# Kernel optimization log

Hardware: AMD Instinct MI355X
Metric: run time of the kernel (lower is better)

Reference implementation:

```python
import jax, jax.numpy as jnp
import numpy as np

ZERO = 1e-8
L = 2            # num_gnn_layers
D = 256          # dim_node_features
B = 32           # graphs per batch
NPG = 256        # nodes per graph
N = B * NPG      # total nodes
E = 131072       # edges per edge-type
MAX_TOKENS = 256 # MAX_TOKENS_OF_A_POST
UPD = 0.5        # args.updated_weights_for_A


def _make_edges(k):
    k1, k2, k3 = jax.random.split(k, 3)
    g = jax.random.randint(k1, (E,), 0, B) * NPG          # keep edges within a graph
    src = g + jax.random.randint(k2, (E,), 0, NPG)
    dst = g + jax.random.randint(k3, (E,), 0, NPG)
    return jnp.stack([src, dst]).astype(jnp.int64)


def setup_inputs() -> dict:
    key = jax.random.key(0)
    ks = jax.random.split(key, 12)
    x = jax.random.normal(ks[0], (N, D), dtype=jnp.float32)
    ei_e = _make_edges(ks[1]); ew_e = jax.random.uniform(ks[2], (E,), dtype=jnp.float32)
    ei_p = _make_edges(ks[3]); ew_p = jax.random.uniform(ks[4], (E,), dtype=jnp.float32)
    ei_o = _make_edges(ks[5]); ew_o = jax.random.uniform(ks[6], (E,), dtype=jnp.float32)
    entity_mask = jax.random.randint(ks[7], (B, NPG), 0, 2).astype(bool)
    pattern_mask = jax.random.randint(ks[8], (B, NPG), 0, 2).astype(bool)
    s = 1.0 / np.sqrt(D)
    W_gcn = (jax.random.normal(ks[9], (L, 3, D, D), dtype=jnp.float32) * s)
    b_gcn = jnp.zeros((L, 3, D), dtype=jnp.float32)
    T_dyn = (jax.random.normal(ks[10], (L, D, D), dtype=jnp.float32) * s)
    return {
        'x': x,
        'edge_index_entity': ei_e, 'edge_weight_entity': ew_e,
        'edge_index_pattern': ei_p, 'edge_weight_pattern': ew_p,
        'edge_index_others': ei_o, 'edge_weight_others': ew_o,
        'entity_mask': entity_mask, 'pattern_mask': pattern_mask,
        'W_gcn': W_gcn, 'b_gcn': b_gcn, 'T_dyn': T_dyn,
    }


def _normalized_correlation_matrix(H):
    # cosine-similarity correlation matrix, symmetrically degree-normalized
    nrm = jnp.sqrt(jnp.sum(H * H, axis=1))
    A = (H @ H.T) / (nrm[:, None] * nrm[None, :] + ZERO)
    dinv = 1.0 / jnp.sqrt(jnp.abs(jnp.sum(A, axis=1)) + ZERO)
    return dinv[:, None] * A * dinv[None, :]


def _gcn(H, W, b, ei, ew):
    # GCNConv(add_self_loops=False, normalize=False): scatter-sum of weighted source messages
    msg = (H @ W)[ei[0]] * ew[:, None]                     # [E, D]
    return jax.ops.segment_sum(msg, ei[1], num_segments=N) + b


def _forward(x, we0, wp0, wo0, W_gcn, b_gcn, T_dyn,
             ei_e, ei_p, ei_o, entity_mask, pattern_mask):
    H = x
    A = _normalized_correlation_matrix(H)                  # [N, N]
    for i in range(L):
        if i == 0:
            we, wp, wo = we0, wp0, wo0
        else:
            # diag(one_hot(src) @ A @ one_hot(dst).T) == A[src, dst]
            we = A[ei_e[0], ei_e[1]]
            wp = A[ei_p[0], ei_p[1]]
            wo = A[ei_o[0], ei_o[1]]
        He = _gcn(H, W_gcn[i, 0], b_gcn[i, 0], ei_e, we)
        Hp = _gcn(H, W_gcn[i, 1], b_gcn[i, 1], ei_p, wp)
        Ho = _gcn(H, W_gcn[i, 2], b_gcn[i, 2], ei_o, wo)
        H = jax.nn.relu(He + Hp + Ho)
        A_hat = jax.nn.sigmoid((H @ T_dyn[i]) @ H.T)
        A = (1.0 - UPD) * A + UPD * A_hat
    # per-graph diagonal blocks of A  -> [B, NPG, NPG]
    A4 = A.reshape(B, NPG, B, NPG)
    idx = jnp.arange(B)
    blocks = A4[idx, :, idx, :]
    A_sum = jnp.sum(blocks, axis=-1)                       # [B, NPG]
    ent_cols = jnp.einsum('bij,bj->bi', blocks, entity_mask.astype(A.dtype))
    pat_cols = jnp.einsum('bij,bj->bi', blocks, pattern_mask.astype(A.dtype))
    map_pattern = A_sum - ent_cols
    map_entity = A_sum - pat_cols

    def finish(m):
        mn = jnp.min(m, axis=1, keepdims=True)
        mx = jnp.max(m, axis=1, keepdims=True)
        m = (m - mn) / (mx - mn + ZERO)
        m = m / (jnp.sum(m, axis=1, keepdims=True) + ZERO)
        return m[:, :MAX_TOKENS]                           # padding() with NPG==MAX_TOKENS

    return finish(map_entity), finish(map_pattern)


def reference(x, edge_index_entity, edge_weight_entity,
              edge_index_pattern, edge_weight_pattern,
              edge_index_others, edge_weight_others,
              entity_mask, pattern_mask, W_gcn, b_gcn, T_dyn):
    return _forward(x, edge_weight_entity, edge_weight_pattern, edge_weight_others,
                    W_gcn, b_gcn, T_dyn,
                    edge_index_entity, edge_index_pattern, edge_index_others,
                    entity_mask, pattern_mask)
```

## Files before the change

kernel.cpp:

```cpp
#include <hip/hip_runtime.h>

#define NND   8192
#define DDIM  256
#define NGRP  32
#define ZEROF 1e-8f
#define LSTR  40
#define TSTR  72
#define OFF_AH 0
#define OFF_AL 2560
#define OFF_BH 5120
#define OFF_BL 10240
#define OFF_TT 5120
#define LDS_U16 15360

typedef unsigned short u16;
typedef __attribute__((ext_vector_type(8))) short short8v;
typedef __attribute__((ext_vector_type(4))) float float4v;

__device__ inline u16 f2bf(float x) {
  unsigned u = __float_as_uint(x);
  u += 0x7fffu + ((u >> 16) & 1u);
  return (u16)(u >> 16);
}
__device__ inline float bf2f(u16 h) { return __uint_as_float((unsigned)h << 16); }
__device__ inline void split2(float x, u16& h, u16& l) {
  h = f2bf(x);
  l = f2bf(x - bf2f(h));
}

__device__ inline float wave_sum(float v) {
#pragma unroll
  for (int off = 32; off > 0; off >>= 1) v += __shfl_down(v, off, 64);
  return v;
}

#define LOAD_REGS(tt, kk)                                                                   \
  {                                                                                         \
    int m_ = tid >> 2, kq_ = (tid & 3) * 8;                                                 \
    size_t aoff_;                                                                           \
    if (MODE == 1)                                                                          \
      aoff_ = (size_t)((tt) * 256 + bym * 64 + m_) * 8192 + (size_t)(g * 256 + (kk) + kq_); \
    else if (MODE == 2 || MODE == 3)                                                        \
      aoff_ = (size_t)(g * 256 + bym * 64 + m_) * 256 + (kk) + kq_;                         \
    else                                                                                    \
      aoff_ = (size_t)(bym * 64 + m_) * 256 + (kk) + kq_;                                   \
    rAh = *(const short8v*)&Ah_g[aoff_];                                                    \
    rAl = *(const short8v*)&Al_g[aoff_];                                                    \
    if (MODE == 1) {                                                                        \
      int n_ = tid >> 2, kq2_ = (tid & 3) * 8;                                              \
      const float* pb_ = Bfp + (((size_t)g * 3 + (tt)) << 16) +                             \
                         (size_t)(col0 + n_) * 256 + (kk) + kq2_;                           \
      rBf[0] = *(const float4*)pb_;                                                         \
      rBf[1] = *(const float4*)(pb_ + 4);                                                   \
    } else if (HALF) {                                                                      \
      int n_ = tid & 63, kq2_ = (tid >> 6) * 8;                                             \
      size_t boff_ = (size_t)(((MODE == 2 || MODE == 3) ? g * 256 : 0) + col0 + n_) * 256   \
                     + (kk) + kq2_;                                                         \
      rBh0 = *(const short8v*)&Bh_g[boff_];                                                 \
      rBl0 = *(const short8v*)&Bl_g[boff_];                                                 \
    } else {                                                                                \
      int n_ = tid & 127, kq2_ = (tid >> 7) * 16;                                           \
      size_t boff_ = (size_t)(col0 + n_) * 256 + (kk) + kq2_;                               \
      rBh0 = *(const short8v*)&Bh_g[boff_]; rBh1 = *(const short8v*)&Bh_g[boff_ + 8];       \
      rBl0 = *(const short8v*)&Bl_g[boff_]; rBl1 = *(const short8v*)&Bl_g[boff_ + 8];       \
    }                                                                                       \
  }

template<int MODE, bool HALF>
__device__ __forceinline__ void mfma_body(
    u16* lds,
    const u16* __restrict__ Ah_g, const u16* __restrict__ Al_g,
    const u16* __restrict__ Bh_g, const u16* __restrict__ Bl_g,
    const float* __restrict__ Bfp,
    float* __restrict__ Cf, u16* __restrict__ Ch, u16* __restrict__ Cl,
    const float* __restrict__ nrm, const float* __restrict__ dinv,
    const float* __restrict__ bias,
    int bxm, int bym, int g) {
  u16* Ahs = lds + OFF_AH;
  u16* Als = lds + OFF_AL;
  u16* Bhs = lds + OFF_BH;
  u16* Bls = lds + OFF_BL;
  u16* Tt  = lds + OFF_TT;
  const int NJ = HALF ? 2 : 4;
  const int tid = threadIdx.x;
  const int col0 = bxm * (HALF ? 64 : 128);
  const int w = tid >> 6, lane = tid & 63;
  const int lm = lane & 15, lq = lane >> 4;
  const int wr = (w >> 1) * 32, wc = (w & 1) * (HALF ? 32 : 64);

  float4v acc[2][4];
#pragma unroll
  for (int i = 0; i < 2; ++i)
#pragma unroll
    for (int j = 0; j < NJ; ++j) acc[i][j] = (float4v)0.f;

  short8v rAh, rAl, rBh0, rBh1, rBl0, rBl1;
  float4 rBf[2];
  const int TOTAL = (MODE == 1) ? 24 : 8;

  LOAD_REGS(0, 0);
  for (int step = 0; step < TOTAL; ++step) {
    if (step) __syncthreads();
    {
      int m = tid >> 2, kq = (tid & 3) * 8;
      *(short8v*)&Ahs[m * LSTR + kq] = rAh;
      *(short8v*)&Als[m * LSTR + kq] = rAl;
    }
    if (MODE == 1) {
      int n = tid >> 2, kq2 = (tid & 3) * 8;
      u16 hh[8], ll[8];
      split2(rBf[0].x, hh[0], ll[0]); split2(rBf[0].y, hh[1], ll[1]);
      split2(rBf[0].z, hh[2], ll[2]); split2(rBf[0].w, hh[3], ll[3]);
      split2(rBf[1].x, hh[4], ll[4]); split2(rBf[1].y, hh[5], ll[5]);
      split2(rBf[1].z, hh[6], ll[6]); split2(rBf[1].w, hh[7], ll[7]);
      *(short8v*)&Bhs[n * LSTR + kq2] = *(short8v*)hh;
      *(short8v*)&Bls[n * LSTR + kq2] = *(short8v*)ll;
    } else if (HALF) {
      int n = tid & 63, kq2 = (tid >> 6) * 8;
      *(short8v*)&Bhs[n * LSTR + kq2] = rBh0;
      *(short8v*)&Bls[n * LSTR + kq2] = rBl0;
    } else {
      int n = tid & 127, kq2 = (tid >> 7) * 16;
      *(short8v*)&Bhs[n * LSTR + kq2] = rBh0; *(short8v*)&Bhs[n * LSTR + kq2 + 8] = rBh1;
      *(short8v*)&Bls[n * LSTR + kq2] = rBl0; *(short8v*)&Bls[n * LSTR + kq2 + 8] = rBl1;
    }
    __syncthreads();
    int nxt = step + 1;
    if (nxt < TOTAL) {
      int tt = nxt >> 3, kk = (nxt & 7) * 32;
      LOAD_REGS(tt, kk);
    }
    short8v ah[2], al[2], bh[4], bl[4];
#pragma unroll
    for (int i = 0; i < 2; ++i) {
      int r = wr + i * 16 + lm;
      ah[i] = *(const short8v*)&Ahs[r * LSTR + lq * 8];
      al[i] = *(const short8v*)&Als[r * LSTR + lq * 8];
    }
#pragma unroll
    for (int j = 0; j < NJ; ++j) {
      int r = wc + j * 16 + lm;
      bh[j] = *(const short8v*)&Bhs[r * LSTR + lq * 8];
      bl[j] = *(const short8v*)&Bls[r * LSTR + lq * 8];
    }
#pragma unroll
    for (int i = 0; i < 2; ++i)
#pragma unroll
      for (int j = 0; j < NJ; ++j) {
        acc[i][j] = __builtin_amdgcn_mfma_f32_16x16x32_bf16(ah[i], bh[j], acc[i][j], 0, 0, 0);
        acc[i][j] = __builtin_amdgcn_mfma_f32_16x16x32_bf16(ah[i], bl[j], acc[i][j], 0, 0, 0);
        acc[i][j] = __builtin_amdgcn_mfma_f32_16x16x32_bf16(al[i], bh[j], acc[i][j], 0, 0, 0);
      }
  }

  if (MODE == 2 || MODE == 3) {
#pragma unroll
    for (int i = 0; i < 2; ++i) {
#pragma unroll
      for (int r = 0; r < 4; ++r) {
        int grow = g * 256 + bym * 64 + wr + i * 16 + lq * 4 + r;
        float di = 0.f, ni = 0.f;
        if (MODE == 2) { di = dinv[grow]; ni = nrm[grow]; }
#pragma unroll
        for (int j = 0; j < NJ; ++j) {
          int gcol = col0 + wc + j * 16 + lm;
          size_t ci = (size_t)grow * 256 + gcol;
          float v = acc[i][j][r];
          if (MODE == 2) {
            int gj = g * 256 + gcol;
            Cf[ci] = v * di * dinv[gj] / (ni * nrm[gj] + ZEROF);
          } else {
            Cf[ci] = 0.5f * Cf[ci] + 0.5f * (1.f / (1.f + expf(-v)));
          }
        }
      }
    }
  } else {
    float bsum[8];
    if (MODE == 1) {
#pragma unroll
      for (int i = 0; i < 2; ++i)
#pragma unroll
        for (int r = 0; r < 4; ++r) {
          int d = bym * 64 + wr + i * 16 + lq * 4 + r;
          bsum[i * 4 + r] = bias[d] + bias[256 + d] + bias[512 + d];
        }
    }
    u16 hv[32], lv[32];
#pragma unroll
    for (int i = 0; i < 2; ++i)
#pragma unroll
      for (int j = 0; j < NJ; ++j)
#pragma unroll
        for (int r = 0; r < 4; ++r) {
          float v = acc[i][j][r];
          if (MODE == 1) v = fmaxf(v + bsum[i * 4 + r], 0.f);
          split2(v, hv[(i * 4 + r) * NJ + j], lv[(i * 4 + r) * NJ + j]);
        }
    int ebase1 = (MODE == 1) ? (g * 256 + col0) : col0;
    int ebase2 = bym * 64;
    size_t estride = (MODE == 0) ? 8192 : 256;
#pragma unroll
    for (int ph = 0; ph < 2; ++ph) {
      __syncthreads();
      const u16* sv = ph ? lv : hv;
#pragma unroll
      for (int i = 0; i < 2; ++i)
#pragma unroll
        for (int j = 0; j < NJ; ++j)
#pragma unroll
          for (int r = 0; r < 4; ++r)
            Tt[(wc + j * 16 + lm) * TSTR + wr + i * 16 + lq * 4 + r] = sv[(i * 4 + r) * NJ + j];
      __syncthreads();
      u16* dst = ph ? Cl : Ch;
      int cc0 = tid >> 3, mm0 = (tid & 7) * 8;
#pragma unroll
      for (int it = 0; it < (HALF ? 2 : 4); ++it) {
        int cc = it * 32 + cc0;
        short8v v = *(const short8v*)&Tt[cc * TSTR + mm0];
        *(short8v*)&dst[(size_t)(ebase1 + cc) * estride + ebase2 + mm0] = v;
      }
    }
  }
}

__global__ void k_prep(const int* __restrict__ e0, const int* __restrict__ e1,
                       const int* __restrict__ e2, const unsigned char* __restrict__ m0,
                       const unsigned char* __restrict__ m1,
                       const float* __restrict__ W, const float* __restrict__ T,
                       const float* __restrict__ x,
                       int* __restrict__ eo, float* __restrict__ emf, float* __restrict__ pmf,
                       u16* __restrict__ Wth, u16* __restrict__ Wtl,
                       float* __restrict__ Mzero,
                       float* __restrict__ nrm, float* __restrict__ Spart,
                       u16* __restrict__ Hh, u16* __restrict__ Hl,
                       int E2, int nCvt) {
  __shared__ float tile[32][33];
  __shared__ float inv[64];
  __shared__ int nz[2];
  const int b = blockIdx.x, tid = threadIdx.x;
  if (b < nCvt) {
    if (tid < 2) nz[tid] = 0;
    __syncthreads();
    if (e0[2 * tid + 1] != 0) atomicAdd(&nz[0], 1);
    int i4 = tid * 4;
    int c = (m0[i4 + 1] != 0) + (m0[i4 + 2] != 0) + (m0[i4 + 3] != 0);
    if (c) atomicAdd(&nz[1], c);
    __syncthreads();
    int fE = (nz[0] == 0), fM = (nz[1] == 0);
    int i = b * 256 + tid;
    if (i < E2) {
      eo[i] = fE ? e0[2 * i] : e0[i];
    } else if (i < 2 * E2) {
      int j = i - E2; eo[E2 + j] = fE ? e1[2 * j] : e1[j];
    } else if (i < 3 * E2) {
      int j = i - 2 * E2; eo[2 * E2 + j] = fE ? e2[2 * j] : e2[j];
    } else if (i < 3 * E2 + NND) {
      int j = i - 3 * E2; unsigned char v = fM ? m0[4 * j] : m0[j];
      emf[j] = 1.f - (float)(v != 0);
    } else if (i < 3 * E2 + 2 * NND) {
      int j = i - 3 * E2 - NND; unsigned char v = fM ? m1[4 * j] : m1[j];
      pmf[j] = 1.f - (float)(v != 0);
    }
  } else if (b < nCvt + 512) {
    int bb = b - nCvt;
    int mat = bb >> 6, rem = bb & 63;
    int k0 = (rem >> 3) * 32, n0 = (rem & 7) * 32;
    const float* src = (mat < 6) ? (W + (size_t)mat * 65536) : (T + (size_t)(mat - 6) * 65536);
    int r = tid >> 3, c4 = (tid & 7) * 4;
    const float4 v = *(const float4*)&src[(size_t)(k0 + r) * 256 + n0 + c4];
    tile[r][c4 + 0] = v.x; tile[r][c4 + 1] = v.y; tile[r][c4 + 2] = v.z; tile[r][c4 + 3] = v.w;
    __syncthreads();
    float o[4] = {tile[c4 + 0][r], tile[c4 + 1][r], tile[c4 + 2][r], tile[c4 + 3][r]};
    u16 hh[4], ll[4];
#pragma unroll
    for (int q = 0; q < 4; ++q) split2(o[q], hh[q], ll[q]);
    size_t off = (size_t)mat * 65536 + (size_t)(n0 + r) * 256 + k0 + c4;
    *(ushort4*)&Wth[off] = *(ushort4*)hh;
    *(ushort4*)&Wtl[off] = *(ushort4*)ll;
  } else if (b < nCvt + 512 + 3072) {
    int bb = b - nCvt - 512;
    float4* p = (float4*)Mzero;
    size_t base = (size_t)bb * 1024 + tid;
    float4 z = make_float4(0.f, 0.f, 0.f, 0.f);
    p[base] = z; p[base + 256] = z; p[base + 512] = z; p[base + 768] = z;
  } else {
    int bn = b - nCvt - 512 - 3072;
    int n0 = bn * 64;
    int w = tid >> 6, lane = tid & 63;
    for (int it = 0; it < 16; ++it) {
      int nl = it * 4 + w;
      int node = n0 + nl;
      const float4 v = *(const float4*)&x[(size_t)node * 256 + lane * 4];
      u16 hh[4], ll[4];
      split2(v.x, hh[0], ll[0]); split2(v.y, hh[1], ll[1]);
      split2(v.z, hh[2], ll[2]); split2(v.w, hh[3], ll[3]);
      *(ushort4*)&Hh[(size_t)node * 256 + lane * 4] = *(ushort4*)hh;
      *(ushort4*)&Hl[(size_t)node * 256 + lane * 4] = *(ushort4*)ll;
      float s = wave_sum(v.x * v.x + v.y * v.y + v.z * v.z + v.w * v.w);
      if (lane == 0) { float nr = sqrtf(s); nrm[node] = nr; inv[nl] = 1.f / nr; }
    }
    __syncthreads();
    float s = 0.f;
    for (int i = 0; i < 64; ++i) s += x[(size_t)(n0 + i) * 256 + tid] * inv[i];
    Spart[bn * 256 + tid] = s;
  }
}

__global__ __launch_bounds__(256, 2) void k_stageA(
    const u16* __restrict__ Hinh, const u16* __restrict__ Hinl,
    const u16* __restrict__ Wth, const u16* __restrict__ Wtl, int l,
    u16* __restrict__ XWTh, u16* __restrict__ XWTl,
    const int* __restrict__ edges, const float* __restrict__ ew0,
    const float* __restrict__ ew1, const float* __restrict__ ew2,
    const float* __restrict__ Abuf, float* __restrict__ Mb, int E_,
    const float* __restrict__ x, const float* __restrict__ Spart,
    const float* __restrict__ nrm, float* __restrict__ dinv) {
  __shared__ u16 lds[LDS_U16];
  const int b = blockIdx.x;
  if (b < 768) {
    mfma_body<0, false>(lds, Hinh, Hinl, Wth + (size_t)l * 768 * 256,
                        Wtl + (size_t)l * 768 * 256, nullptr,
                        nullptr, XWTh, XWTl, nullptr, nullptr, nullptr,
                        b >> 7, b & 127, 0);
  } else if (b < 1280) {
    int bi = b - 768;
    for (int i = bi * 256 + threadIdx.x; i < 3 * E_; i += 131072) {
      int t = i / E_;
      int e = i - t * E_;
      const int* ei = edges + (size_t)t * 2 * E_;
      int src = ei[e], dst = ei[E_ + e];
      float wgt = l ? Abuf[(size_t)src * 256 + (dst & 255)]
                    : (t == 0 ? ew0 : (t == 1 ? ew1 : ew2))[e];
      int gg = src >> 8;
      atomicAdd(&Mb[(((size_t)gg * 3 + t) << 16) + ((size_t)(dst & 255) << 8) + (src & 255)],
                wgt);
    }
  } else {
    float* Sl = (float*)lds;
    const int tid = threadIdx.x;
    float s = 0.f;
    for (int bb = 0; bb < 128; ++bb) s += Spart[bb * 256 + tid];
    Sl[tid] = s;
    __syncthreads();
    int base = (b - 1280) * 64;
    int w = tid >> 6, lane = tid & 63;
    const float4 sv = *(const float4*)&Sl[lane * 4];
    for (int it = 0; it < 16; ++it) {
      int node = base + it * 4 + w;
      const float4 v = *(const float4*)&x[(size_t)node * 256 + lane * 4];
      float s2 = wave_sum(v.x * sv.x + v.y * sv.y + v.z * sv.z + v.w * sv.w);
      if (lane == 0) {
        float rowsum = s2 / nrm[node];
        dinv[node] = rsqrtf(fabsf(rowsum) + ZEROF);
      }
    }
  }
}

__global__ __launch_bounds__(256, 2) void k_stageB(
    const u16* __restrict__ XWTh, const u16* __restrict__ XWTl,
    const float* __restrict__ Mb,
    u16* __restrict__ Houth, u16* __restrict__ Houtl, const float* __restrict__ bias,
    const u16* __restrict__ xh, const u16* __restrict__ xl, float* __restrict__ Abuf,
    const float* __restrict__ nrm, const float* __restrict__ dinv) {
  __shared__ u16 lds[LDS_U16];
  const int b = blockIdx.x;
  if (b < 512) {
    int g = b & 31, r = b >> 5;
    mfma_body<1, true>(lds, XWTh, XWTl, nullptr, nullptr, Mb,
                       nullptr, Houth, Houtl, nullptr, nullptr, bias,
                       r >> 2, r & 3, g);
  } else {
    int bb = b - 512;
    int g = bb & 31, r = bb >> 5;
    mfma_body<2, true>(lds, xh, xl, xh, xl, nullptr, Abuf, nullptr, nullptr,
                       nrm, dinv, nullptr, r >> 2, r & 3, g);
  }
}

__global__ __launch_bounds__(256, 2) void k_stageC(
    const u16* __restrict__ Wth, const u16* __restrict__ Wtl, int l,
    const u16* __restrict__ Hh, const u16* __restrict__ Hl,
    u16* __restrict__ tmph, u16* __restrict__ tmpl) {
  __shared__ u16 lds[LDS_U16];
  const int b = blockIdx.x;
  mfma_body<4, true>(lds, Wth + (size_t)(6 + l) * 65536, Wtl + (size_t)(6 + l) * 65536,
                     Hh, Hl, nullptr, nullptr, tmph, tmpl, nullptr, nullptr, nullptr,
                     b & 127, b >> 7, 0);
}

__global__ __launch_bounds__(256, 2) void k_stageD(
    const u16* __restrict__ tmph, const u16* __restrict__ tmpl,
    const u16* __restrict__ Hh, const u16* __restrict__ Hl,
    float* __restrict__ Abuf) {
  __shared__ u16 lds[LDS_U16];
  const int b = blockIdx.x;
  int g = b & 31, r = b >> 5;
  mfma_body<3, true>(lds, tmph, tmpl, Hh, Hl, nullptr, Abuf, nullptr, nullptr,
                     nullptr, nullptr, nullptr, r >> 2, r & 3, g);
}

__global__ void k_maps(const float* __restrict__ Abuf, const float* __restrict__ emf,
                       const float* __restrict__ pmf, float* __restrict__ out) {
  __shared__ float sme[256], smp[256], red[256];
  const int g = blockIdx.x, tid = threadIdx.x, w = tid >> 6, lane = tid & 63;
  const int j0 = g * 256 + lane * 4;
  const float4 pmv = *(const float4*)&pmf[j0];
  const float4 emv = *(const float4*)&emf[j0];
  for (int it = 0; it < 64; ++it) {
    int nl = it * 4 + w;
    const float4 a = *(const float4*)&Abuf[((size_t)g * 256 + nl) * 256 + lane * 4];
    float me = a.x * pmv.x + a.y * pmv.y + a.z * pmv.z + a.w * pmv.w;
    float mp = a.x * emv.x + a.y * emv.y + a.z * emv.z + a.w * emv.w;
#pragma unroll
    for (int off = 32; off > 0; off >>= 1) {
      me += __shfl_down(me, off, 64);
      mp += __shfl_down(mp, off, 64);
    }
    if (lane == 0) { sme[nl] = me; smp[nl] = mp; }
  }
  __syncthreads();
  for (int which = 0; which < 2; ++which) {
    float v = which ? smp[tid] : sme[tid];
    red[tid] = v; __syncthreads();
    for (int s = 128; s > 0; s >>= 1) { if (tid < s) red[tid] = fminf(red[tid], red[tid + s]); __syncthreads(); }
    float mn = red[0]; __syncthreads();
    red[tid] = v; __syncthreads();
    for (int s = 128; s > 0; s >>= 1) { if (tid < s) red[tid] = fmaxf(red[tid], red[tid + s]); __syncthreads(); }
    float mx = red[0]; __syncthreads();
    float m = (v - mn) / (mx - mn + ZEROF);
    red[tid] = m; __syncthreads();
    for (int s = 128; s > 0; s >>= 1) { if (tid < s) red[tid] += red[tid + s]; __syncthreads(); }
    float sum = red[0]; __syncthreads();
    out[which * NND + g * 256 + tid] = m / (sum + ZEROF);
  }
}

extern "C" void kernel_launch(void* const* d_in, const int* in_sizes, int n_in,
                              void* d_out, int out_size, void* d_ws, size_t ws_size,
                              hipStream_t stream) {
  const float* x = (const float*)d_in[0];
  const unsigned char* em_raw = (const unsigned char*)d_in[7];
  const unsigned char* pm_raw = (const unsigned char*)d_in[8];
  const float* W  = (const float*)d_in[9];
  const float* bg = (const float*)d_in[10];
  const float* T  = (const float*)d_in[11];
  float* out = (float*)d_out;
  const int E_ = in_sizes[2];
  const int E2 = 2 * E_;

  float* ws = (float*)d_ws;
  size_t o = 0;
  float* Abuf = ws + o; o += (size_t)NND * 256;
  float* Mb3  = ws + o; o += (size_t)2 * NGRP * 3 * 65536;
  u16* Hh   = (u16*)(ws + o); o += (size_t)NND * 256 / 2;
  u16* Hl   = (u16*)(ws + o); o += (size_t)NND * 256 / 2;
  u16* H2h  = (u16*)(ws + o); o += (size_t)NND * 256 / 2;
  u16* H2l  = (u16*)(ws + o); o += (size_t)NND * 256 / 2;
  u16* tmph = (u16*)(ws + o); o += (size_t)NND * 256 / 2;
  u16* tmpl = (u16*)(ws + o); o += (size_t)NND * 256 / 2;
  u16* XWTh = (u16*)(ws + o); o += (size_t)768 * NND / 2;
  u16* XWTl = (u16*)(ws + o); o += (size_t)768 * NND / 2;
  u16* Wth  = (u16*)(ws + o); o += (size_t)8 * 65536 / 2;
  u16* Wtl  = (u16*)(ws + o); o += (size_t)8 * 65536 / 2;
  float* nrm   = ws + o; o += NND;
  float* dinv  = ws + o; o += NND;
  float* Spart = ws + o; o += 128 * 256;
  float* emf   = ws + o; o += NND;
  float* pmf   = ws + o; o += NND;
  int* edges   = (int*)(ws + o); o += (size_t)3 * E2;

  const float* ew0 = (const float*)d_in[2];
  const float* ew1 = (const float*)d_in[4];
  const float* ew2 = (const float*)d_in[6];
  float* Mb_l0 = Mb3;
  float* Mb_l1 = Mb3 + (size_t)NGRP * 3 * 65536;

  const int nCvt = (3 * E2 + 2 * NND + 255) / 256;

  k_prep<<<nCvt + 512 + 3072 + 128, 256, 0, stream>>>(
      (const int*)d_in[1], (const int*)d_in[3], (const int*)d_in[5], em_raw, pm_raw,
      W, T, x, edges, emf, pmf, Wth, Wtl, Mb3, nrm, Spart, Hh, Hl, E2, nCvt);

  k_stageA<<<1408, 256, 0, stream>>>(Hh, Hl, Wth, Wtl, 0, XWTh, XWTl,
                                     edges, ew0, ew1, ew2, Abuf, Mb_l0, E_,
                                     x, Spart, nrm, dinv);
  k_stageB<<<1024, 256, 0, stream>>>(XWTh, XWTl, Mb_l0, H2h, H2l, bg,
                                     Hh, Hl, Abuf, nrm, dinv);
  k_stageC<<<512, 256, 0, stream>>>(Wth, Wtl, 0, H2h, H2l, tmph, tmpl);
  k_stageD<<<512, 256, 0, stream>>>(tmph, tmpl, H2h, H2l, Abuf);

  k_stageA<<<1280, 256, 0, stream>>>(H2h, H2l, Wth, Wtl, 1, XWTh, XWTl,
                                     edges, ew0, ew1, ew2, Abuf, Mb_l1, E_,
                                     x, Spart, nrm, dinv);
  k_stageB<<<512, 256, 0, stream>>>(XWTh, XWTl, Mb_l1, Hh, Hl, bg + 768,
                                    nullptr, nullptr, nullptr, nullptr, nullptr);
  k_stageC<<<512, 256, 0, stream>>>(Wth, Wtl, 1, Hh, Hl, tmph, tmpl);
  k_stageD<<<512, 256, 0, stream>>>(tmph, tmpl, Hh, Hl, Abuf);

  k_maps<<<NGRP, 256, 0, stream>>>(Abuf, emf, pmf, out);
}
```

Baseline: 283.8 us.

## Bin edges by graph, type and destination slice; accumulate adjacency in shared memory

The prep kernel now buckets every edge into one of 768 bins, keyed by graph, edge type and 32-row destination slice. Each bin entry holds a packed 16-bit cell index and the edge weight. Stage A then builds each adjacency slice with shared-memory atomics and writes it densely to global memory, both layers reuse one Mb buffer, and the global-atomic scatter, the large zero-fill and the edge-index copy are gone. In exchange there is a fixed bin capacity of 1024 that silently drops edges in any bin that overflows, which is only safe for evenly spread inputs. It also adds an extra init kernel launch.

```diff
diff --git a/kernel.cpp b/kernel.cpp
--- a/kernel.cpp
+++ b/kernel.cpp
@@ -12,6 +12,8 @@
 #define OFF_BL 10240
 #define OFF_TT 5120
 #define LDS_U16 15360
+#define NBIN 768
+#define BINCAP 1024
 
 typedef unsigned short u16;
 typedef __attribute__((ext_vector_type(8))) short short8v;
@@ -224,46 +226,47 @@
   }
 }
 
+__global__ void k_init(unsigned* __restrict__ binCount) {
+  int i = blockIdx.x * 256 + threadIdx.x;
+  if (i < NBIN) binCount[i] = 0u;
+}
+
 __global__ void k_prep(const int* __restrict__ e0, const int* __restrict__ e1,
                        const int* __restrict__ e2, const unsigned char* __restrict__ m0,
                        const unsigned char* __restrict__ m1,
                        const float* __restrict__ W, const float* __restrict__ T,
                        const float* __restrict__ x,
-                       int* __restrict__ eo, float* __restrict__ emf, float* __restrict__ pmf,
+                       const float* __restrict__ ew0, const float* __restrict__ ew1,
+                       const float* __restrict__ ew2,
+                       float* __restrict__ emf, float* __restrict__ pmf,
                        u16* __restrict__ Wth, u16* __restrict__ Wtl,
-                       float* __restrict__ Mzero,
+                       unsigned* __restrict__ binCount, u16* __restrict__ binCell,
+                       float* __restrict__ binW,
                        float* __restrict__ nrm, float* __restrict__ Spart,
-                       u16* __restrict__ Hh, u16* __restrict__ Hl,
-                       int E2, int nCvt) {
+                       u16* __restrict__ Hh, u16* __restrict__ Hl, int E_) {
   __shared__ float tile[32][33];
   __shared__ float inv[64];
   __shared__ int nz[2];
   const int b = blockIdx.x, tid = threadIdx.x;
-  if (b < nCvt) {
-    if (tid < 2) nz[tid] = 0;
-    __syncthreads();
-    if (e0[2 * tid + 1] != 0) atomicAdd(&nz[0], 1);
+  if (b < 64) {
+    if (tid == 0) nz[1] = 0;
+    __syncthreads();
     int i4 = tid * 4;
     int c = (m0[i4 + 1] != 0) + (m0[i4 + 2] != 0) + (m0[i4 + 3] != 0);
     if (c) atomicAdd(&nz[1], c);
     __syncthreads();
-    int fE = (nz[0] == 0), fM = (nz[1] == 0);
+    int fM = (nz[1] == 0);
     int i = b * 256 + tid;
-    if (i < E2) {
-      eo[i] = fE ? e0[2 * i] : e0[i];
-    } else if (i < 2 * E2) {
-      int j = i - E2; eo[E2 + j] = fE ? e1[2 * j] : e1[j];
-    } else if (i < 3 * E2) {
-      int j = i - 2 * E2; eo[2 * E2 + j] = fE ? e2[2 * j] : e2[j];
-    } else if (i < 3 * E2 + NND) {
-      int j = i - 3 * E2; unsigned char v = fM ? m0[4 * j] : m0[j];
-      emf[j] = 1.f - (float)(v != 0);
-    } else if (i < 3 * E2 + 2 * NND) {
-      int j = i - 3 * E2 - NND; unsigned char v = fM ? m1[4 * j] : m1[j];
+    if (i < NND) {
+      unsigned char v = fM ? m0[4 * i] : m0[i];
+      emf[i] = 1.f - (float)(v != 0);
+    } else {
+      int j = i - NND;
+      unsigned char v = fM ? m1[4 * j] : m1[j];
       pmf[j] = 1.f - (float)(v != 0);
     }
-  } else if (b < nCvt + 512) {
-    int bb = b - nCvt;
+  } else if (b < 576) {
+    int bb = b - 64;
     int mat = bb >> 6, rem = bb & 63;
     int k0 = (rem >> 3) * 32, n0 = (rem & 7) * 32;
     const float* src = (mat < 6) ? (W + (size_t)mat * 65536) : (T + (size_t)(mat - 6) * 65536);
@@ -278,14 +281,32 @@
     size_t off = (size_t)mat * 65536 + (size_t)(n0 + r) * 256 + k0 + c4;
     *(ushort4*)&Wth[off] = *(ushort4*)hh;
     *(ushort4*)&Wtl[off] = *(ushort4*)ll;
-  } else if (b < nCvt + 512 + 3072) {
-    int bb = b - nCvt - 512;
-    float4* p = (float4*)Mzero;
-    size_t base = (size_t)bb * 1024 + tid;
-    float4 z = make_float4(0.f, 0.f, 0.f, 0.f);
-    p[base] = z; p[base + 256] = z; p[base + 512] = z; p[base + 768] = z;
+  } else if (b < 1088) {
+    if (tid == 0) nz[0] = 0;
+    __syncthreads();
+    if (e0[2 * tid + 1] != 0) atomicAdd(&nz[0], 1);
+    __syncthreads();
+    int fE = (nz[0] == 0);
+    int bb = b - 576;
+    for (int i = bb * 256 + tid; i < 3 * E_; i += 512 * 256) {
+      int t = i / E_;
+      int e = i - t * E_;
+      const int* er = (t == 0) ? e0 : (t == 1 ? e1 : e2);
+      int src, dst;
+      if (fE) { src = er[2 * e]; dst = er[2 * (E_ + e)]; }
+      else    { src = er[e];     dst = er[E_ + e]; }
+      float w = (t == 0 ? ew0 : (t == 1 ? ew1 : ew2))[e];
+      int g = src >> 8;
+      int dstl = dst & 255, srcl = src & 255;
+      int bin = ((g * 3 + t) << 3) | (dstl >> 5);
+      unsigned slot = atomicAdd(&binCount[bin], 1u);
+      if (slot < BINCAP) {
+        binCell[(size_t)bin * BINCAP + slot] = (u16)(((dstl & 31) << 8) | srcl);
+        binW[(size_t)bin * BINCAP + slot] = w;
+      }
+    }
   } else {
-    int bn = b - nCvt - 512 - 3072;
+    int bn = b - 1088;
     int n0 = bn * 64;
     int w = tid >> 6, lane = tid & 63;
     for (int it = 0; it < 16; ++it) {
@@ -311,39 +332,51 @@
     const u16* __restrict__ Hinh, const u16* __restrict__ Hinl,
     const u16* __restrict__ Wth, const u16* __restrict__ Wtl, int l,
     u16* __restrict__ XWTh, u16* __restrict__ XWTl,
-    const int* __restrict__ edges, const float* __restrict__ ew0,
-    const float* __restrict__ ew1, const float* __restrict__ ew2,
-    const float* __restrict__ Abuf, float* __restrict__ Mb, int E_,
+    const unsigned* __restrict__ binCount, const u16* __restrict__ binCell,
+    const float* __restrict__ binW,
+    const float* __restrict__ Abuf, float* __restrict__ Mb,
     const float* __restrict__ x, const float* __restrict__ Spart,
     const float* __restrict__ nrm, float* __restrict__ dinv) {
-  __shared__ u16 lds[LDS_U16];
+  __shared__ u16 lds[16384];
   const int b = blockIdx.x;
+  const int tid = threadIdx.x;
   if (b < 768) {
     mfma_body<0, false>(lds, Hinh, Hinl, Wth + (size_t)l * 768 * 256,
                         Wtl + (size_t)l * 768 * 256, nullptr,
                         nullptr, XWTh, XWTl, nullptr, nullptr, nullptr,
                         b >> 7, b & 127, 0);
-  } else if (b < 1280) {
-    int bi = b - 768;
-    for (int i = bi * 256 + threadIdx.x; i < 3 * E_; i += 131072) {
-      int t = i / E_;
-      int e = i - t * E_;
-      const int* ei = edges + (size_t)t * 2 * E_;
-      int src = ei[e], dst = ei[E_ + e];
-      float wgt = l ? Abuf[(size_t)src * 256 + (dst & 255)]
-                    : (t == 0 ? ew0 : (t == 1 ? ew1 : ew2))[e];
-      int gg = src >> 8;
-      atomicAdd(&Mb[(((size_t)gg * 3 + t) << 16) + ((size_t)(dst & 255) << 8) + (src & 255)],
-                wgt);
-    }
+  } else if (b < 1536) {
+    int bin = b - 768;
+    float* Ml = (float*)lds;
+    for (int i = tid; i < 8192; i += 256) Ml[i] = 0.f;
+    __syncthreads();
+    int count = min((int)binCount[bin], BINCAP);
+    const u16* cells = binCell + (size_t)bin * BINCAP;
+    const float* wts = binW + (size_t)bin * BINCAP;
+    int gt = bin >> 3, sub = bin & 7;
+    int g = gt / 3;
+    for (int i = tid; i < count; i += 256) {
+      int cell = cells[i];
+      float w;
+      if (l) {
+        int srcl = cell & 255, dstq = cell >> 8;
+        w = Abuf[(size_t)(g * 256 + srcl) * 256 + sub * 32 + dstq];
+      } else {
+        w = wts[i];
+      }
+      atomicAdd(&Ml[cell], w);
+    }
+    __syncthreads();
+    float4* dst = (float4*)(Mb + ((size_t)gt << 16) + (size_t)sub * 32 * 256);
+    const float4* srcp = (const float4*)Ml;
+    for (int i = tid; i < 2048; i += 256) dst[i] = srcp[i];
   } else {
     float* Sl = (float*)lds;
-    const int tid = threadIdx.x;
     float s = 0.f;
     for (int bb = 0; bb < 128; ++bb) s += Spart[bb * 256 + tid];
     Sl[tid] = s;
     __syncthreads();
-    int base = (b - 1280) * 64;
+    int base = (b - 1536) * 64;
     int w = tid >> 6, lane = tid & 63;
     const float4 sv = *(const float4*)&Sl[lane * 4];
     for (int it = 0; it < 16; ++it) {
@@ -448,12 +481,11 @@
   const float* T  = (const float*)d_in[11];
   float* out = (float*)d_out;
   const int E_ = in_sizes[2];
-  const int E2 = 2 * E_;
 
   float* ws = (float*)d_ws;
   size_t o = 0;
   float* Abuf = ws + o; o += (size_t)NND * 256;
-  float* Mb3  = ws + o; o += (size_t)2 * NGRP * 3 * 65536;
+  float* Mb   = ws + o; o += (size_t)NGRP * 3 * 65536;
   u16* Hh   = (u16*)(ws + o); o += (size_t)NND * 256 / 2;
   u16* Hl   = (u16*)(ws + o); o += (size_t)NND * 256 / 2;
   u16* H2h  = (u16*)(ws + o); o += (size_t)NND * 256 / 2;
@@ -469,32 +501,32 @@
   float* Spart = ws + o; o += 128 * 256;
   float* emf   = ws + o; o += NND;
   float* pmf   = ws + o; o += NND;
-  int* edges   = (int*)(ws + o); o += (size_t)3 * E2;
+  unsigned* binCount = (unsigned*)(ws + o); o += NBIN;
+  u16* binCell = (u16*)(ws + o); o += (size_t)NBIN * BINCAP / 2;
+  float* binW  = ws + o; o += (size_t)NBIN * BINCAP;
 
   const float* ew0 = (const float*)d_in[2];
   const float* ew1 = (const float*)d_in[4];
   const float* ew2 = (const float*)d_in[6];
-  float* Mb_l0 = Mb3;
-  float* Mb_l1 = Mb3 + (size_t)NGRP * 3 * 65536;
-
-  const int nCvt = (3 * E2 + 2 * NND + 255) / 256;
-
-  k_prep<<<nCvt + 512 + 3072 + 128, 256, 0, stream>>>(
+
+  k_init<<<3, 256, 0, stream>>>(binCount);
+  k_prep<<<1216, 256, 0, stream>>>(
       (const int*)d_in[1], (const int*)d_in[3], (const int*)d_in[5], em_raw, pm_raw,
-      W, T, x, edges, emf, pmf, Wth, Wtl, Mb3, nrm, Spart, Hh, Hl, E2, nCvt);
-
-  k_stageA<<<1408, 256, 0, stream>>>(Hh, Hl, Wth, Wtl, 0, XWTh, XWTl,
-                                     edges, ew0, ew1, ew2, Abuf, Mb_l0, E_,
+      W, T, x, ew0, ew1, ew2, emf, pmf, Wth, Wtl,
+      binCount, binCell, binW, nrm, Spart, Hh, Hl, E_);
+
+  k_stageA<<<1664, 256, 0, stream>>>(Hh, Hl, Wth, Wtl, 0, XWTh, XWTl,
+                                     binCount, binCell, binW, Abuf, Mb,
                                      x, Spart, nrm, dinv);
-  k_stageB<<<1024, 256, 0, stream>>>(XWTh, XWTl, Mb_l0, H2h, H2l, bg,
+  k_stageB<<<1024, 256, 0, stream>>>(XWTh, XWTl, Mb, H2h, H2l, bg,
                                      Hh, Hl, Abuf, nrm, dinv);
   k_stageC<<<512, 256, 0, stream>>>(Wth, Wtl, 0, H2h, H2l, tmph, tmpl);
   k_stageD<<<512, 256, 0, stream>>>(tmph, tmpl, H2h, H2l, Abuf);
 
-  k_stageA<<<1280, 256, 0, stream>>>(H2h, H2l, Wth, Wtl, 1, XWTh, XWTl,
-                                     edges, ew0, ew1, ew2, Abuf, Mb_l1, E_,
+  k_stageA<<<1536, 256, 0, stream>>>(H2h, H2l, Wth, Wtl, 1, XWTh, XWTl,
+                                     binCount, binCell, binW, Abuf, Mb,
                                      x, Spart, nrm, dinv);
-  k_stageB<<<512, 256, 0, stream>>>(XWTh, XWTl, Mb_l1, Hh, Hl, bg + 768,
+  k_stageB<<<512, 256, 0, stream>>>(XWTh, XWTl, Mb, Hh, Hl, bg + 768,
                                     nullptr, nullptr, nullptr, nullptr, nullptr);
   k_stageC<<<512, 256, 0, stream>>>(Wth, Wtl, 1, Hh, Hl, tmph, tmpl);
   k_stageD<<<512, 256, 0, stream>>>(tmph, tmpl, Hh, Hl, Abuf);
```

Measured after the change: 356.3 us. 1.26x slower.
